# Performance work log

Measured on AMD Instinct MI355X. Metric: run time of the kernel, lower is better.

The kernel has to match this reference:

```python
import jax, jax.numpy as jnp
import numpy as np


def _ens_linear(x, W, b):
    # x: [B,T,Din], W: [E,Din,Dout], b: [E,Dout] -> [E,B,T,Dout]
    return jnp.einsum('btd,edh->ebth', x, W) + b[:, None, None, :]


def _gilr_scan(v, f):
    # h_t = f_t * h_{t-1} + (1 - f_t) * v_t, h_0 = 0 (tie-input-gate linear recurrence)
    def comb(c1, c2):
        a1, b1 = c1
        a2, b2 = c2
        return a2 * a1, a2 * b1 + b2
    _, h = jax.lax.associative_scan(comb, (f, (1.0 - f) * v), axis=1)
    return h


def setup_inputs() -> dict:
    key = jax.random.key(0)
    ks = jax.random.split(key, 7)
    B, T, Din, D = 8, 4096, 512, 512
    x = jax.random.normal(ks[0], (B, T, Din), dtype=jnp.float32)
    s_in = 1.0 / np.sqrt(Din)
    s = 1.0 / np.sqrt(D)
    W_in = jax.random.uniform(ks[1], (2, Din, D), jnp.float32, -s_in, s_in)
    b_in = jax.random.uniform(ks[2], (2, D), jnp.float32, -s_in, s_in)
    W_mid = jax.random.uniform(ks[3], (4, D, D), jnp.float32, -s, s)
    b_mid = jax.random.uniform(ks[4], (4, D), jnp.float32, -s, s)
    W_out = jax.random.uniform(ks[5], (D, D), jnp.float32, -s, s)
    b_out = jax.random.uniform(ks[6], (D,), jnp.float32, -s, s)
    return {"x": x, "W_in": W_in, "b_in": b_in, "W_mid": W_mid,
            "b_mid": b_mid, "W_out": W_out, "b_out": b_out}


def reference(x, W_in, b_in, W_mid, b_mid, W_out, b_out):
    # in_proj (ensemble of 2): u[0] -> v, u[1] -> f
    u = _ens_linear(x, W_in, b_in)
    v = jnp.tanh(u[0])
    f = jax.nn.sigmoid(u[1])
    # first gated linear recurrence (hidden_pre starts at zeros)
    v = _gilr_scan(v, f)
    hidden_pre = v[:, -1:, :]
    # middle_proj (ensemble of 4): f, i, o, z
    u = _ens_linear(v, W_mid, b_mid)
    f2 = jax.nn.sigmoid(u[0])
    i = jax.nn.sigmoid(u[1])
    o = jax.nn.sigmoid(u[2])
    z = jnp.tanh(u[3])
    # second gated linear recurrence (hidden_middle starts at zeros)
    out = _gilr_scan(i * z, f2)
    hidden_middle = out[:, -1:, :]
    out = out * o
    out = out @ W_out + b_out
    hidden = jnp.concatenate((hidden_pre, hidden_middle), axis=-1)
    hidden = jnp.transpose(hidden, (1, 0, 2))  # [1, B, 2D]
    return out, hidden
```

## Files before the change

### kernel.cpp

```cpp
#include <hip/hip_runtime.h>

typedef short short8 __attribute__((ext_vector_type(8)));
typedef float float4v __attribute__((ext_vector_type(4)));
typedef unsigned short u16;
typedef unsigned int u32;

#define T_LEN 4096
#define DDIM 512
#define BATCH 8
#define MROWS 32768
#define CH 32
#define NC 128

__device__ __forceinline__ u16 f2b(float x) {
    unsigned u = __float_as_uint(x);
    unsigned r = (u + 0x7FFFu + ((u >> 16) & 1u)) >> 16;
    return (u16)r;
}
__device__ __forceinline__ float b2f(u16 h) {
    return __uint_as_float((u32)h << 16);
}
__device__ __forceinline__ float sigm(float x) {
    return __builtin_amdgcn_rcpf(1.f + __builtin_amdgcn_exp2f(-1.44269504f * x));
}
__device__ __forceinline__ float tanh_fast(float x) {
    return 1.f - 2.f * __builtin_amdgcn_rcpf(1.f + __builtin_amdgcn_exp2f(2.88539008f * x));
}

__device__ __forceinline__ void gl2lds16(const u16* g, u16* l) {
    __builtin_amdgcn_global_load_lds(
        (const __attribute__((address_space(1))) void*)g,
        (__attribute__((address_space(3))) void*)l, 16, 0, 0);
}

__global__ __launch_bounds__(256) void cvt_x(const float* __restrict__ x,
                                             u16* __restrict__ xb, size_t n) {
    size_t i = ((size_t)blockIdx.x * 256 + threadIdx.x) * 4;
    if (i < n) {
        float4v v = *(const float4v*)&x[i];
        ushort4 p;
        p.x = f2b(v[0]); p.y = f2b(v[1]); p.z = f2b(v[2]); p.w = f2b(v[3]);
        *(ushort4*)&xb[i] = p;
    }
}

template <int MODE>
__global__ __launch_bounds__(256) void cvt_wt(const float* __restrict__ W,
                                              u16* __restrict__ Wt, int N) {
    int idx = blockIdx.x * 256 + threadIdx.x;
    if (idx >= N * 512) return;
    int j = idx >> 9;
    int k = idx & 511;
    int gate, d;
    if (MODE == 1) { gate = (j >> 4) & 1; d = (j >> 5) * 16 + (j & 15); }
    else if (MODE == 2) { gate = (j >> 4) & 3; d = (j >> 6) * 16 + (j & 15); }
    else { gate = 0; d = j; }
    Wt[(size_t)j * 512 + k] = f2b(W[((size_t)gate * 512 + k) * 512 + d]);
}

template <int MODE>
__global__ __launch_bounds__(512, 4) void gemm_act(
    const u16* __restrict__ A, const u16* __restrict__ Bt,
    const float* __restrict__ bias, void* __restrict__ o0v,
    void* __restrict__ o1v, void* __restrict__ o2v) {
    constexpr int K = 512;
    constexpr int BK = 32;
    constexpr int NKT = K / BK;
    constexpr int LBA = 256 * 32;
    constexpr int LBB = 128 * 32;
    constexpr int GX = (MODE == 1) ? 8 : (MODE == 2) ? 16 : 4;
    constexpr int NWG = 128 * GX;
    __shared__ u16 lsA[3][LBA];
    __shared__ u16 lsB[3][LBB];
    const int tid = threadIdx.x;
    const int lane = tid & 63;
    const int wid = tid >> 6;
    const int wr = wid >> 1;
    const int wc = wid & 1;
    const int l0 = lane & 15, lh = lane >> 4;

    const int h = blockIdx.x;
    const int l = (h & 7) * (NWG / 8) + (h >> 3);
    const int bn0 = (l & (GX - 1)) * 128;
    const int bm0 = (l / GX) * 256;

    float4v acc[4][4];
#pragma unroll
    for (int m = 0; m < 4; ++m)
#pragma unroll
        for (int n = 0; n < 4; ++n) acc[m][n] = (float4v){0.f, 0.f, 0.f, 0.f};

    int growA[2], gchA[2], growB, gchB;
#pragma unroll
    for (int i = 0; i < 2; ++i) {
        int flat = i * 512 + tid;
        growA[i] = flat >> 2;
        gchA[i] = (((flat & 3) ^ ((growA[i] >> 1) & 3))) * 8;
    }
    growB = tid >> 2;
    gchB = (((tid & 3) ^ ((growB >> 1) & 3))) * 8;

#define STAGE(buf, kt)                                                        \
    {                                                                         \
        const int k0 = (kt) * BK;                                             \
        _Pragma("unroll") for (int i = 0; i < 2; ++i)                         \
            gl2lds16(&A[(size_t)(bm0 + growA[i]) * K + k0 + gchA[i]],         \
                     &lsA[buf][(i * 512 + tid) * 8]);                         \
        gl2lds16(&Bt[(size_t)(bn0 + growB) * K + k0 + gchB],                  \
                 &lsB[buf][tid * 8]);                                         \
    }

    STAGE(0, 0);
    STAGE(1, 1);

    for (int kt = 0; kt < NKT; ++kt) {
        const int cur = kt % 3;
        if (kt + 1 < NKT)
            asm volatile("s_waitcnt vmcnt(3)" ::: "memory");
        else
            asm volatile("s_waitcnt vmcnt(0)" ::: "memory");
        __builtin_amdgcn_s_barrier();
        __builtin_amdgcn_sched_barrier(0);
        if (kt + 2 < NKT) STAGE((kt + 2) % 3, kt + 2);
        short8 af[4], bf[4];
#pragma unroll
        for (int m = 0; m < 4; ++m) {
            int r = wr * 64 + m * 16 + l0;
            af[m] = *(const short8*)&lsA[cur][r * 32 + ((lh ^ ((r >> 1) & 3)) * 8)];
        }
#pragma unroll
        for (int n = 0; n < 4; ++n) {
            int r = wc * 64 + n * 16 + l0;
            bf[n] = *(const short8*)&lsB[cur][r * 32 + ((lh ^ ((r >> 1) & 3)) * 8)];
        }
        asm volatile("s_waitcnt lgkmcnt(0)" ::: "memory");
        __builtin_amdgcn_sched_barrier(0);
        __builtin_amdgcn_s_setprio(1);
#pragma unroll
        for (int m = 0; m < 4; ++m)
#pragma unroll
            for (int n = 0; n < 4; ++n)
                acc[m][n] = __builtin_amdgcn_mfma_f32_16x16x32_bf16(
                    af[m], bf[n], acc[m][n], 0, 0, 0);
        __builtin_amdgcn_s_setprio(0);
    }
#undef STAGE

    if (MODE == 3) {
#pragma unroll
        for (int m = 0; m < 4; ++m) {
#pragma unroll
            for (int n = 0; n < 4; ++n) {
                int col = bn0 + wc * 64 + n * 16 + l0;
                float bv = bias[col];
#pragma unroll
                for (int r = 0; r < 4; ++r) {
                    int rw = bm0 + wr * 64 + m * 16 + lh * 4 + r;
                    ((float*)o0v)[(size_t)rw * 512 + col] = acc[m][n][r] + bv;
                }
            }
        }
    } else if (MODE == 1) {
        const int base5 = (bn0 + wc * 64) >> 5;
#pragma unroll
        for (int p = 0; p < 2; ++p) {
            const int d = (base5 + p) * 16 + l0;
            const float bvv = bias[d], bvf = bias[512 + d];
#pragma unroll
            for (int m = 0; m < 4; ++m) {
#pragma unroll
                for (int r = 0; r < 4; ++r) {
                    int rw = bm0 + wr * 64 + m * 16 + lh * 4 + r;
                    float f1 = sigm(acc[m][2 * p + 1][r] + bvf);
                    float g = (1.f - f1) * tanh_fast(acc[m][2 * p][r] + bvv);
                    size_t oidx = (size_t)rw * 512 + d;
                    ((u16*)o0v)[oidx] = f2b(f1);
                    ((u16*)o1v)[oidx] = f2b(g);
                }
            }
        }
    } else {
        const int d = ((bn0 + wc * 64) >> 6) * 16 + l0;
        const float bv0 = bias[d], bv1 = bias[512 + d];
        const float bv2 = bias[1024 + d], bv3 = bias[1536 + d];
#pragma unroll
        for (int m = 0; m < 4; ++m) {
#pragma unroll
            for (int r = 0; r < 4; ++r) {
                int rw = bm0 + wr * 64 + m * 16 + lh * 4 + r;
                float f2 = sigm(acc[m][0][r] + bv0);
                float ii = sigm(acc[m][1][r] + bv1);
                float oo = sigm(acc[m][2][r] + bv2);
                float zz = tanh_fast(acc[m][3][r] + bv3);
                float g = (1.f - f2) * ii * zz;
                size_t oidx = (size_t)rw * 512 + d;
                ((u16*)o0v)[oidx] = f2b(f2);
                ((u16*)o1v)[oidx] = f2b(g);
                ((u16*)o2v)[oidx] = f2b(oo);
            }
        }
    }
}

__global__ __launch_bounds__(128) void scan_p1(const u16* __restrict__ f,
                                               const u16* __restrict__ g,
                                               float* __restrict__ cA,
                                               float* __restrict__ cB) {
    int d0 = threadIdx.x * 4;
    int c = blockIdx.x & (NC - 1);
    int b = blockIdx.x >> 7;
    size_t base = ((size_t)b * T_LEN + c * CH) * DDIM + d0;
    float Aa[4] = {1.f, 1.f, 1.f, 1.f}, Bb[4] = {0.f, 0.f, 0.f, 0.f};
    for (int t = 0; t < CH; ++t) {
        ushort4 fq = *(const ushort4*)&f[base];
        ushort4 gq = *(const ushort4*)&g[base];
        float ff[4] = {b2f(fq.x), b2f(fq.y), b2f(fq.z), b2f(fq.w)};
        float gg[4] = {b2f(gq.x), b2f(gq.y), b2f(gq.z), b2f(gq.w)};
#pragma unroll
        for (int j = 0; j < 4; ++j) {
            Bb[j] = ff[j] * Bb[j] + gg[j];
            Aa[j] *= ff[j];
        }
        base += DDIM;
    }
    size_t ci = (size_t)c * 4096 + b * DDIM + d0;
#pragma unroll
    for (int j = 0; j < 4; ++j) {
        cA[ci + j] = Aa[j];
        cB[ci + j] = Bb[j];
    }
}

__global__ __launch_bounds__(256) void scan_p2(float* __restrict__ cA,
                                               const float* __restrict__ cB) {
    int ln = blockIdx.x * 256 + threadIdx.x;
    float h = 0.f;
    for (int c = 0; c < NC; ++c) {
        size_t ix = (size_t)c * 4096 + ln;
        float a = cA[ix], bb = cB[ix];
        cA[ix] = h;
        h = a * h + bb;
    }
}

template <int S>
__global__ __launch_bounds__(128) void scan_p3(
    const u16* __restrict__ f, const u16* __restrict__ g,
    const u16* __restrict__ o, const float* __restrict__ cA,
    u16* __restrict__ hb, float* __restrict__ hid) {
    int d0 = threadIdx.x * 4;
    int c = blockIdx.x & (NC - 1);
    int b = blockIdx.x >> 7;
    size_t base = ((size_t)b * T_LEN + c * CH) * DDIM + d0;
    size_t ci = (size_t)c * 4096 + b * DDIM + d0;
    float h[4] = {cA[ci], cA[ci + 1], cA[ci + 2], cA[ci + 3]};
    for (int t = 0; t < CH; ++t) {
        ushort4 fq = *(const ushort4*)&f[base];
        ushort4 gq = *(const ushort4*)&g[base];
        float ff[4] = {b2f(fq.x), b2f(fq.y), b2f(fq.z), b2f(fq.w)};
        float gg[4] = {b2f(gq.x), b2f(gq.y), b2f(gq.z), b2f(gq.w)};
        float w[4];
#pragma unroll
        for (int j = 0; j < 4; ++j) {
            h[j] = ff[j] * h[j] + gg[j];
            w[j] = h[j];
        }
        if (S == 2) {
            ushort4 oq = *(const ushort4*)&o[base];
            w[0] *= b2f(oq.x); w[1] *= b2f(oq.y);
            w[2] *= b2f(oq.z); w[3] *= b2f(oq.w);
        }
        ushort4 p;
        p.x = f2b(w[0]); p.y = f2b(w[1]); p.z = f2b(w[2]); p.w = f2b(w[3]);
        *(ushort4*)&hb[base] = p;
        base += DDIM;
    }
    if (c == NC - 1) {
#pragma unroll
        for (int j = 0; j < 4; ++j)
            hid[b * 1024 + (S == 1 ? 0 : 512) + d0 + j] = h[j];
    }
}

extern "C" void kernel_launch(void* const* d_in, const int* in_sizes, int n_in,
                              void* d_out, int out_size, void* d_ws,
                              size_t ws_size, hipStream_t stream) {
    const float* x = (const float*)d_in[0];
    const float* W_in = (const float*)d_in[1];
    const float* b_in = (const float*)d_in[2];
    const float* W_mid = (const float*)d_in[3];
    const float* b_mid = (const float*)d_in[4];
    const float* W_out = (const float*)d_in[5];
    const float* b_out = (const float*)d_in[6];
    float* out = (float*)d_out;
    char* ws = (char*)d_ws;

    const size_t MB = 1u << 20;
    const size_t MD = (size_t)MROWS * DDIM;

    u16* wt_in = (u16*)(ws);
    u16* wt_mid = (u16*)(ws + 1 * MB);
    u16* wt_out = (u16*)(ws + 3 * MB);
    u16* hb = (u16*)(ws + 4 * MB);
    u16* S0 = (u16*)(ws + 36 * MB);
    u16* S1 = (u16*)(ws + 68 * MB);
    u16* S2 = (u16*)(ws + 100 * MB);
    float* cA = (float*)(ws + 164 * MB);
    float* cB = (float*)(ws + 166 * MB);
    float* hid = out + MD;

    cvt_x<<<(int)(MD / 4 / 256), 256, 0, stream>>>(x, hb, MD);
    cvt_wt<1><<<(1024 * 512) / 256, 256, 0, stream>>>(W_in, wt_in, 1024);
    cvt_wt<2><<<(2048 * 512) / 256, 256, 0, stream>>>(W_mid, wt_mid, 2048);
    cvt_wt<3><<<(512 * 512) / 256, 256, 0, stream>>>(W_out, wt_out, 512);

    gemm_act<1><<<1024, 512, 0, stream>>>(hb, wt_in, b_in, S0, S1, nullptr);
    scan_p1<<<1024, 128, 0, stream>>>(S0, S1, cA, cB);
    scan_p2<<<16, 256, 0, stream>>>(cA, cB);
    scan_p3<1><<<1024, 128, 0, stream>>>(S0, S1, nullptr, cA, hb, hid);

    gemm_act<2><<<2048, 512, 0, stream>>>(hb, wt_mid, b_mid, S0, S1, S2);
    scan_p1<<<1024, 128, 0, stream>>>(S0, S1, cA, cB);
    scan_p2<<<16, 256, 0, stream>>>(cA, cB);
    scan_p3<2><<<1024, 128, 0, stream>>>(S0, S1, S2, cA, hb, hid);

    gemm_act<3><<<512, 512, 0, stream>>>(hb, wt_out, b_out, out, nullptr,
                                         nullptr);
}
```

Measured before the change: 259.7 us.

## Fuse chunk-level scan reduction into GEMM epilogue, drop scan_p1 kernels

The GEMM epilogue now composes each 32-timestep chunk's (A,B) scan carry from the fp32 gate values it already holds in registers. It combines lanes with xor shuffles and writes the chunk summaries directly to cA/cB. This removes the two scan_p1 launches and their re-read of the bf16 f/g tensors from global memory. The carries are now computed from unrounded fp32 values while scan_p3 uses the bf16-rounded ones, which adds a small numerical mismatch and some extra epilogue work and register pressure.

```diff
diff --git a/kernel.cpp b/kernel.cpp
--- a/kernel.cpp
+++ b/kernel.cpp
@@ -31,6 +31,16 @@
     __builtin_amdgcn_global_load_lds(
         (const __attribute__((address_space(1))) void*)g,
         (__attribute__((address_space(3))) void*)l, 16, 0, 0);
+}
+
+__device__ __forceinline__ void compose_xor(float& A, float& B, int mask,
+                                            bool selfIsHi) {
+    float pa = __shfl_xor(A, mask);
+    float pb = __shfl_xor(B, mask);
+    float loA = selfIsHi ? pa : A, loB = selfIsHi ? pb : B;
+    float hiA = selfIsHi ? A : pa, hiB = selfIsHi ? B : pb;
+    A = hiA * loA;
+    B = hiA * loB + hiB;
 }
 
 __global__ __launch_bounds__(256) void cvt_x(const float* __restrict__ x,
@@ -62,7 +72,8 @@
 __global__ __launch_bounds__(512, 4) void gemm_act(
     const u16* __restrict__ A, const u16* __restrict__ Bt,
     const float* __restrict__ bias, void* __restrict__ o0v,
-    void* __restrict__ o1v, void* __restrict__ o2v) {
+    void* __restrict__ o1v, void* __restrict__ o2v,
+    float* __restrict__ cA, float* __restrict__ cB) {
     constexpr int K = 512;
     constexpr int BK = 32;
     constexpr int NKT = K / BK;
@@ -160,14 +171,22 @@
                 }
             }
         }
-    } else if (MODE == 1) {
+        return;
+    }
+
+    const int bb = bm0 >> 12;
+    const int tq = (bm0 & 4095) + wr * 64;
+
+    if (MODE == 1) {
         const int base5 = (bn0 + wc * 64) >> 5;
 #pragma unroll
         for (int p = 0; p < 2; ++p) {
             const int d = (base5 + p) * 16 + l0;
             const float bvv = bias[d], bvf = bias[512 + d];
+            float segA[4], segB[4];
 #pragma unroll
             for (int m = 0; m < 4; ++m) {
+                float Ap = 1.f, Bp = 0.f;
 #pragma unroll
                 for (int r = 0; r < 4; ++r) {
                     int rw = bm0 + wr * 64 + m * 16 + lh * 4 + r;
@@ -176,15 +195,34 @@
                     size_t oidx = (size_t)rw * 512 + d;
                     ((u16*)o0v)[oidx] = f2b(f1);
                     ((u16*)o1v)[oidx] = f2b(g);
+                    Bp = f1 * Bp + g;
+                    Ap *= f1;
                 }
+                segA[m] = Ap; segB[m] = Bp;
+            }
+#pragma unroll
+            for (int m = 0; m < 4; ++m) {
+                compose_xor(segA[m], segB[m], 16, (lh & 1) != 0);
+                compose_xor(segA[m], segB[m], 32, (lh & 2) != 0);
+            }
+            if (lh == 0) {
+                float c0A = segA[1] * segA[0], c0B = segA[1] * segB[0] + segB[1];
+                float c1A = segA[3] * segA[2], c1B = segA[3] * segB[2] + segB[3];
+                int c0 = tq >> 5;
+                size_t ci0 = (size_t)c0 * 4096 + bb * 512 + d;
+                size_t ci1 = ci0 + 4096;
+                cA[ci0] = c0A; cB[ci0] = c0B;
+                cA[ci1] = c1A; cB[ci1] = c1B;
             }
         }
     } else {
         const int d = ((bn0 + wc * 64) >> 6) * 16 + l0;
         const float bv0 = bias[d], bv1 = bias[512 + d];
         const float bv2 = bias[1024 + d], bv3 = bias[1536 + d];
+        float segA[4], segB[4];
 #pragma unroll
         for (int m = 0; m < 4; ++m) {
+            float Ap = 1.f, Bp = 0.f;
 #pragma unroll
             for (int r = 0; r < 4; ++r) {
                 int rw = bm0 + wr * 64 + m * 16 + lh * 4 + r;
@@ -197,37 +235,25 @@
                 ((u16*)o0v)[oidx] = f2b(f2);
                 ((u16*)o1v)[oidx] = f2b(g);
                 ((u16*)o2v)[oidx] = f2b(oo);
-            }
-        }
-    }
-}
-
-__global__ __launch_bounds__(128) void scan_p1(const u16* __restrict__ f,
-                                               const u16* __restrict__ g,
-                                               float* __restrict__ cA,
-                                               float* __restrict__ cB) {
-    int d0 = threadIdx.x * 4;
-    int c = blockIdx.x & (NC - 1);
-    int b = blockIdx.x >> 7;
-    size_t base = ((size_t)b * T_LEN + c * CH) * DDIM + d0;
-    float Aa[4] = {1.f, 1.f, 1.f, 1.f}, Bb[4] = {0.f, 0.f, 0.f, 0.f};
-    for (int t = 0; t < CH; ++t) {
-        ushort4 fq = *(const ushort4*)&f[base];
-        ushort4 gq = *(const ushort4*)&g[base];
-        float ff[4] = {b2f(fq.x), b2f(fq.y), b2f(fq.z), b2f(fq.w)};
-        float gg[4] = {b2f(gq.x), b2f(gq.y), b2f(gq.z), b2f(gq.w)};
-#pragma unroll
-        for (int j = 0; j < 4; ++j) {
-            Bb[j] = ff[j] * Bb[j] + gg[j];
-            Aa[j] *= ff[j];
-        }
-        base += DDIM;
-    }
-    size_t ci = (size_t)c * 4096 + b * DDIM + d0;
-#pragma unroll
-    for (int j = 0; j < 4; ++j) {
-        cA[ci + j] = Aa[j];
-        cB[ci + j] = Bb[j];
+                Bp = f2 * Bp + g;
+                Ap *= f2;
+            }
+            segA[m] = Ap; segB[m] = Bp;
+        }
+#pragma unroll
+        for (int m = 0; m < 4; ++m) {
+            compose_xor(segA[m], segB[m], 16, (lh & 1) != 0);
+            compose_xor(segA[m], segB[m], 32, (lh & 2) != 0);
+        }
+        if (lh == 0) {
+            float c0A = segA[1] * segA[0], c0B = segA[1] * segB[0] + segB[1];
+            float c1A = segA[3] * segA[2], c1B = segA[3] * segB[2] + segB[3];
+            int c0 = tq >> 5;
+            size_t ci0 = (size_t)c0 * 4096 + bb * 512 + d;
+            size_t ci1 = ci0 + 4096;
+            cA[ci0] = c0A; cB[ci0] = c0B;
+            cA[ci1] = c1A; cB[ci1] = c1B;
+        }
     }
 }
 
@@ -314,16 +340,16 @@
     cvt_wt<2><<<(2048 * 512) / 256, 256, 0, stream>>>(W_mid, wt_mid, 2048);
     cvt_wt<3><<<(512 * 512) / 256, 256, 0, stream>>>(W_out, wt_out, 512);
 
-    gemm_act<1><<<1024, 512, 0, stream>>>(hb, wt_in, b_in, S0, S1, nullptr);
-    scan_p1<<<1024, 128, 0, stream>>>(S0, S1, cA, cB);
+    gemm_act<1><<<1024, 512, 0, stream>>>(hb, wt_in, b_in, S0, S1, nullptr,
+                                          cA, cB);
     scan_p2<<<16, 256, 0, stream>>>(cA, cB);
     scan_p3<1><<<1024, 128, 0, stream>>>(S0, S1, nullptr, cA, hb, hid);
 
-    gemm_act<2><<<2048, 512, 0, stream>>>(hb, wt_mid, b_mid, S0, S1, S2);
-    scan_p1<<<1024, 128, 0, stream>>>(S0, S1, cA, cB);
+    gemm_act<2><<<2048, 512, 0, stream>>>(hb, wt_mid, b_mid, S0, S1, S2,
+                                          cA, cB);
     scan_p2<<<16, 256, 0, stream>>>(cA, cB);
     scan_p3<2><<<1024, 128, 0, stream>>>(S0, S1, S2, cA, hb, hid);
 
     gemm_act<3><<<512, 512, 0, stream>>>(hb, wt_out, b_out, out, nullptr,
-                                         nullptr);
-}
+                                         nullptr, nullptr, nullptr);
+}
```

Measured after the change: 244.0 us. 6.1% less time.
